# Kernel optimization log

Hardware: AMD Instinct MI355X
Metric: run time of the kernel (lower is better)

## Reference

```python
import jax, jax.numpy as jnp
import numpy as np

B, S, D = 4, 2048, 1024
H, DK, DV = 16, 64, 64
GRAPH_ATTN_BIAS = 2.0
POS_WIN = 4.0
LN_EPS = 1e-6


def setup_inputs() -> dict:
    key = jax.random.key(0)
    ks = jax.random.split(key, 9)
    init = 0.02
    return {
        "q": jax.random.normal(ks[0], (B, S, D), jnp.float32),
        "k": jax.random.normal(ks[1], (B, S, D), jnp.float32),
        "v": jax.random.normal(ks[2], (B, S, D), jnp.float32),
        "Wq": jax.random.normal(ks[3], (D, H * DK), jnp.float32) * init,
        "Wk": jax.random.normal(ks[4], (D, H * DK), jnp.float32) * init,
        "Wv": jax.random.normal(ks[5], (D, H * DV), jnp.float32) * init,
        "Wfc": jax.random.normal(ks[6], (H * DV, D), jnp.float32) * init,
        "gamma": jnp.ones((D,), jnp.float32),
        "beta": jnp.zeros((D,), jnp.float32),
    }


def reference(q, k, v, Wq, Wk, Wv, Wfc, gamma, beta):
    b, sq, d = q.shape
    sk = k.shape[1]
    residual = q
    # projections -> [b, s, h, dk]
    qh = (q @ Wq).reshape(b, sq, H, DK)
    kh = (k @ Wk).reshape(b, sk, H, DK)
    vh = (v @ Wv).reshape(b, sk, H, DV)
    # scaled dot-product scores: [b, h, sq, sk]
    attn = jnp.einsum("bqhd,bkhd->bhqk", qh / jnp.sqrt(jnp.float32(DK)), kh)
    # gaussian graph bias (constant additive logit bias, applied pre-softmax)
    gaussian_w = -0.5 * GRAPH_ATTN_BIAS ** 2 / (0.5 * POS_WIN) ** 2
    attn = attn + gaussian_w
    weights = jax.nn.softmax(attn, axis=-1)
    out = jnp.einsum("bhqk,bkhd->bqhd", weights, vh).reshape(b, sq, H * DV)
    out = out @ Wfc + residual
    # layer norm over last dim, eps=1e-6
    mu = jnp.mean(out, axis=-1, keepdims=True)
    var = jnp.mean((out - mu) ** 2, axis=-1, keepdims=True)
    out = (out - mu) * jax.lax.rsqrt(var + LN_EPS) * gamma + beta
    return out
```

## Files before the change

kernel.cpp:

```cpp
#include <hip/hip_runtime.h>

typedef __attribute__((ext_vector_type(4))) float f32x4;
typedef __attribute__((ext_vector_type(8))) __bf16 bf16x8;

#define MFMA16(a, b, c) __builtin_amdgcn_mfma_f32_16x16x32_bf16(a, b, c, 0, 0, 0)

__device__ __forceinline__ void gload_lds16(const void* g, void* l) {
  __builtin_amdgcn_global_load_lds(
      (const __attribute__((address_space(1))) unsigned int*)g,
      (__attribute__((address_space(3))) unsigned int*)l, 16, 0, 0);
}

__global__ __launch_bounds__(256) void cvt3(
    const float* __restrict__ q, const float* __restrict__ k, const float* __restrict__ v,
    __bf16* __restrict__ qb, __bf16* __restrict__ kb, __bf16* __restrict__ vb) {
  const float* src;
  __bf16* dst;
  if (blockIdx.y == 0) { src = q; dst = qb; }
  else if (blockIdx.y == 1) { src = k; dst = kb; }
  else { src = v; dst = vb; }
  size_t i = ((size_t)blockIdx.x * 256 + threadIdx.x) * 8;
  float4 a = *(const float4*)(src + i);
  float4 b = *(const float4*)(src + i + 4);
  struct alignas(16) B8 { __bf16 h[8]; } ob;
  ob.h[0] = (__bf16)a.x; ob.h[1] = (__bf16)a.y; ob.h[2] = (__bf16)a.z; ob.h[3] = (__bf16)a.w;
  ob.h[4] = (__bf16)b.x; ob.h[5] = (__bf16)b.y; ob.h[6] = (__bf16)b.z; ob.h[7] = (__bf16)b.w;
  *(B8*)(dst + i) = ob;
}

__global__ __launch_bounds__(256) void wtrans(const float* __restrict__ W,
                                              __bf16* __restrict__ Wt) {
  __shared__ float T[64][65];
  int t = threadIdx.x;
  int tc = blockIdx.x, tr = blockIdx.y;
#pragma unroll
  for (int i = 0; i < 4; i++) {
    int r = i * 16 + (t >> 4), c = (t & 15) * 4;
    float4 x = *(const float4*)(W + (size_t)(tr * 64 + r) * 1024 + tc * 64 + c);
    T[r][c] = x.x; T[r][c + 1] = x.y; T[r][c + 2] = x.z; T[r][c + 3] = x.w;
  }
  __syncthreads();
#pragma unroll
  for (int i = 0; i < 4; i++) {
    int r = i * 16 + (t >> 4), c = (t & 15) * 4;
    struct alignas(8) B4 { __bf16 h[4]; } ob;
#pragma unroll
    for (int j = 0; j < 4; j++) ob.h[j] = (__bf16)T[c + j][r];
    *(B4*)(Wt + (size_t)(tc * 64 + r) * 1024 + tr * 64 + c) = ob;
  }
}

template <int MODE>
__global__ __launch_bounds__(256) void gemm_bt(
    const __bf16* __restrict__ A, const __bf16* __restrict__ Bt,
    const float* __restrict__ resid, __bf16* __restrict__ outb,
    float* __restrict__ outf) {
  constexpr int K = 1024;
  __shared__ __align__(16) __bf16 As[128 * 32];
  __shared__ __align__(16) __bf16 Bs[128 * 32];
  int t = threadIdx.x, lane = t & 63, w = t >> 6;
  int l15 = lane & 15, l4 = lane >> 4;
  int m0 = blockIdx.y * 128, n0 = blockIdx.x * 128;
  int wr = w >> 1, wc = w & 1;

  f32x4 z = {0.f, 0.f, 0.f, 0.f};
  f32x4 acc[4][4];
#pragma unroll
  for (int mi = 0; mi < 4; mi++)
#pragma unroll
    for (int ni = 0; ni < 4; ni++) acc[mi][ni] = z;

  int rA = t >> 2, cA = (t & 3) * 8;

  for (int kt = 0; kt < K / 32; ++kt) {
    __syncthreads();
    int k0 = kt * 32;
#pragma unroll
    for (int i = 0; i < 2; i++) {
      gload_lds16(A + (size_t)(m0 + i * 64 + rA) * K + k0 + cA, As + (i * 4 + w) * 512);
      gload_lds16(Bt + (size_t)(n0 + i * 64 + rA) * K + k0 + cA, Bs + (i * 4 + w) * 512);
    }
    __syncthreads();

    bf16x8 af[4], bfr[4];
#pragma unroll
    for (int mi = 0; mi < 4; mi++)
      af[mi] = *(const bf16x8*)(As + (wr * 64 + mi * 16 + l15) * 32 + l4 * 8);
#pragma unroll
    for (int ni = 0; ni < 4; ni++)
      bfr[ni] = *(const bf16x8*)(Bs + (wc * 64 + ni * 16 + l15) * 32 + l4 * 8);
#pragma unroll
    for (int mi = 0; mi < 4; mi++)
#pragma unroll
      for (int ni = 0; ni < 4; ni++)
        acc[mi][ni] = MFMA16(af[mi], bfr[ni], acc[mi][ni]);
  }

#pragma unroll
  for (int mi = 0; mi < 4; mi++)
#pragma unroll
    for (int ni = 0; ni < 4; ni++)
#pragma unroll
      for (int r = 0; r < 4; r++) {
        int row = m0 + wr * 64 + mi * 16 + l4 * 4 + r;
        int col = n0 + wc * 64 + ni * 16 + l15;
        if (MODE == 0) {
          int b = row >> 11, s = row & 2047, h = col >> 6, dk = col & 63;
          outb[(((size_t)b * 16 + h) * 2048 + s) * 64 + dk] = (__bf16)acc[mi][ni][r];
        } else if (MODE == 2) {
          int bh = ((row >> 11) << 4) + (col >> 6);
          outb[((size_t)bh * 64 + (col & 63)) * 2048 + (row & 2047)] = (__bf16)acc[mi][ni][r];
        } else {
          size_t idx = (size_t)row * 1024 + col;
          outf[idx] = acc[mi][ni][r] + resid[idx];
        }
      }
}

__global__ __launch_bounds__(256) void attn_fwd3(
    const __bf16* __restrict__ QH, const __bf16* __restrict__ KH,
    const __bf16* __restrict__ VHt, __bf16* __restrict__ AO) {
  constexpr int S = 2048;
  int bid = blockIdx.x;
  int bh = bid & 63;
  int qt = bid >> 6;
  int t = threadIdx.x, lane = t & 63, w = t >> 6;
  int l15 = lane & 15, l4 = lane >> 4;

  __shared__ __align__(16) __bf16 Ks[2][64 * 64];
  __shared__ __align__(16) __bf16 Vs[2][64 * 64];
  __shared__ __align__(16) __bf16 Ps[4][16 * 64];

  char* myP = (char*)&Ps[w][0];

  const __bf16* Qp = QH + ((size_t)bh * S + qt * 64 + w * 16) * 64;
  const __bf16* Kp = KH + (size_t)bh * S * 64;
  const __bf16* Vp = VHt + (size_t)bh * 64 * S;

  int srow = lane >> 3;
  int sce = ((lane & 7) ^ srow) * 8;

  bf16x8 aq[2];
#pragma unroll
  for (int ks = 0; ks < 2; ks++) {
    bf16x8 x = *(const bf16x8*)(Qp + l15 * 64 + ks * 32 + l4 * 8);
#pragma unroll
    for (int j = 0; j < 8; j++) x[j] = (__bf16)((float)x[j] * 0.125f);
    aq[ks] = x;
  }

  f32x4 z = {0.f, 0.f, 0.f, 0.f};
  f32x4 o[4];
  float mr[4], lr[4];
#pragma unroll
  for (int r = 0; r < 4; r++) { o[r] = z; mr[r] = -1e30f; lr[r] = 0.f; }

#pragma unroll
  for (int i = 0; i < 2; i++) {
    int r = (i * 4 + w) * 8 + srow;
    gload_lds16(Kp + (size_t)r * 64 + sce, &Ks[0][(i * 4 + w) * 512]);
    gload_lds16(Vp + (size_t)r * S + sce, &Vs[0][(i * 4 + w) * 512]);
  }
  __syncthreads();

  for (int kt = 0; kt < 32; ++kt) {
    int cur = kt & 1;
    if (kt < 31) {
#pragma unroll
      for (int i = 0; i < 2; i++) {
        int r = (i * 4 + w) * 8 + srow;
        gload_lds16(Kp + (size_t)((kt + 1) * 64 + r) * 64 + sce,
                    &Ks[cur ^ 1][(i * 4 + w) * 512]);
        gload_lds16(Vp + (size_t)r * S + (kt + 1) * 64 + sce,
                    &Vs[cur ^ 1][(i * 4 + w) * 512]);
      }
    }

    const char* kbuf = (const char*)&Ks[cur][0];
    const char* vbuf = (const char*)&Vs[cur][0];

    bf16x8 kv[2][4];
#pragma unroll
    for (int ks = 0; ks < 2; ks++)
#pragma unroll
      for (int nf = 0; nf < 4; nf++) {
        int row = nf * 16 + l15;
        int cb = (ks * 64 + l4 * 16) ^ ((row & 7) << 4);
        kv[ks][nf] = *(const bf16x8*)(kbuf + row * 128 + cb);
      }

    f32x4 s4[4];
#pragma unroll
    for (int nf = 0; nf < 4; nf++) s4[nf] = z;
#pragma unroll
    for (int ks = 0; ks < 2; ks++)
#pragma unroll
      for (int nf = 0; nf < 4; nf++)
        s4[nf] = MFMA16(aq[ks], kv[ks][nf], s4[nf]);

#pragma unroll
    for (int ks = 0; ks < 2; ks++)
#pragma unroll
      for (int nf = 0; nf < 4; nf++) {
        int row = nf * 16 + l15;
        int cb = (ks * 64 + l4 * 16) ^ ((row & 7) << 4);
        kv[ks][nf] = *(const bf16x8*)(vbuf + row * 128 + cb);
      }

    float pm[4];
#pragma unroll
    for (int r = 0; r < 4; r++) {
      float v0 = fmaxf(fmaxf(s4[0][r], s4[1][r]), fmaxf(s4[2][r], s4[3][r]));
#pragma unroll
      for (int d = 1; d < 16; d <<= 1) v0 = fmaxf(v0, __shfl_xor(v0, d));
      pm[r] = v0;
    }
    float need = fmaxf(fmaxf(pm[0] - mr[0], pm[1] - mr[1]),
                       fmaxf(pm[2] - mr[2], pm[3] - mr[3]));
    if (__any(need > 8.0f)) {
#pragma unroll
      for (int r = 0; r < 4; r++) {
        float mn = fmaxf(mr[r], pm[r]);
        float corr = __expf(mr[r] - mn);
        mr[r] = mn;
        lr[r] *= corr;
#pragma unroll
        for (int nf = 0; nf < 4; nf++) o[nf][r] *= corr;
      }
    }
    float rs[4] = {0.f, 0.f, 0.f, 0.f};
#pragma unroll
    for (int nf = 0; nf < 4; nf++)
#pragma unroll
      for (int r = 0; r < 4; r++) {
        float p = __expf(s4[nf][r] - mr[r]);
        rs[r] += p;
        int rowb = l4 * 4 + r;
        int cb = (nf * 32 + l15 * 2) ^ ((rowb & 7) << 4);
        *(__bf16*)(myP + rowb * 128 + cb) = (__bf16)p;
      }
#pragma unroll
    for (int r = 0; r < 4; r++) {
      float v0 = rs[r];
#pragma unroll
      for (int d = 1; d < 16; d <<= 1) v0 += __shfl_xor(v0, d);
      lr[r] += v0;
    }

    bf16x8 ap[2];
#pragma unroll
    for (int ks = 0; ks < 2; ks++) {
      int cb = (ks * 64 + l4 * 16) ^ ((l15 & 7) << 4);
      ap[ks] = *(const bf16x8*)(myP + l15 * 128 + cb);
    }

#pragma unroll
    for (int ks = 0; ks < 2; ks++)
#pragma unroll
      for (int nf = 0; nf < 4; nf++)
        o[nf] = MFMA16(ap[ks], kv[ks][nf], o[nf]);

    __syncthreads();
  }

  int b = bh >> 4, h = bh & 15;
#pragma unroll
  for (int nf = 0; nf < 4; nf++)
#pragma unroll
    for (int r = 0; r < 4; r++) {
      int row = qt * 64 + w * 16 + l4 * 4 + r;
      int col = h * 64 + nf * 16 + l15;
      AO[((size_t)b * S + row) * 1024 + col] = (__bf16)(o[nf][r] / lr[r]);
    }
}

__global__ __launch_bounds__(256) void ln_inplace(float* __restrict__ X,
                                                  const float* __restrict__ gamma,
                                                  const float* __restrict__ beta) {
  int row = blockIdx.x, t = threadIdx.x;
  int w = t >> 6, lane = t & 63;
  float4 x = *(const float4*)(X + (size_t)row * 1024 + t * 4);
  float s = x.x + x.y + x.z + x.w;
#pragma unroll
  for (int d = 1; d < 64; d <<= 1) s += __shfl_xor(s, d);
  __shared__ float red1[4];
  __shared__ float red2[4];
  if (lane == 0) red1[w] = s;
  __syncthreads();
  float mean = (red1[0] + red1[1] + red1[2] + red1[3]) * (1.0f / 1024.0f);
  float4 d4;
  d4.x = x.x - mean; d4.y = x.y - mean; d4.z = x.z - mean; d4.w = x.w - mean;
  float sq = d4.x * d4.x + d4.y * d4.y + d4.z * d4.z + d4.w * d4.w;
#pragma unroll
  for (int d = 1; d < 64; d <<= 1) sq += __shfl_xor(sq, d);
  if (lane == 0) red2[w] = sq;
  __syncthreads();
  float var = (red2[0] + red2[1] + red2[2] + red2[3]) * (1.0f / 1024.0f);
  float rstd = rsqrtf(var + 1e-6f);
  float4 g = *(const float4*)(gamma + t * 4);
  float4 be = *(const float4*)(beta + t * 4);
  float4 oo;
  oo.x = d4.x * rstd * g.x + be.x;
  oo.y = d4.y * rstd * g.y + be.y;
  oo.z = d4.z * rstd * g.z + be.z;
  oo.w = d4.w * rstd * g.w + be.w;
  *(float4*)(X + (size_t)row * 1024 + t * 4) = oo;
}

extern "C" void kernel_launch(void* const* d_in, const int* in_sizes, int n_in,
                              void* d_out, int out_size, void* d_ws, size_t ws_size,
                              hipStream_t stream) {
  (void)in_sizes; (void)n_in; (void)out_size; (void)ws_size;
  const float* q = (const float*)d_in[0];
  const float* k = (const float*)d_in[1];
  const float* v = (const float*)d_in[2];
  const float* Wq = (const float*)d_in[3];
  const float* Wk = (const float*)d_in[4];
  const float* Wv = (const float*)d_in[5];
  const float* Wfc = (const float*)d_in[6];
  const float* gamma = (const float*)d_in[7];
  const float* beta = (const float*)d_in[8];
  float* out = (float*)d_out;

  const size_t MB = 1ull << 20;
  char* ws = (char*)d_ws;
  __bf16* qb = (__bf16*)(ws + 0 * MB);
  __bf16* kb = (__bf16*)(ws + 16 * MB);
  __bf16* vb = (__bf16*)(ws + 32 * MB);
  __bf16* QH = (__bf16*)(ws + 48 * MB);
  __bf16* KH = (__bf16*)(ws + 64 * MB);
  __bf16* VHt = (__bf16*)(ws + 80 * MB);
  __bf16* Wqt = (__bf16*)(ws + 96 * MB);
  __bf16* Wkt = (__bf16*)(ws + 98 * MB);
  __bf16* Wvt = (__bf16*)(ws + 100 * MB);
  __bf16* Wfct = (__bf16*)(ws + 102 * MB);
  __bf16* AO = qb;

  cvt3<<<dim3(4096, 3), 256, 0, stream>>>(q, k, v, qb, kb, vb);
  wtrans<<<dim3(16, 16), 256, 0, stream>>>(Wq, Wqt);
  wtrans<<<dim3(16, 16), 256, 0, stream>>>(Wk, Wkt);
  wtrans<<<dim3(16, 16), 256, 0, stream>>>(Wv, Wvt);
  wtrans<<<dim3(16, 16), 256, 0, stream>>>(Wfc, Wfct);

  gemm_bt<0><<<dim3(8, 64), 256, 0, stream>>>(qb, Wqt, nullptr, QH, nullptr);
  gemm_bt<0><<<dim3(8, 64), 256, 0, stream>>>(kb, Wkt, nullptr, KH, nullptr);
  gemm_bt<2><<<dim3(8, 64), 256, 0, stream>>>(vb, Wvt, nullptr, VHt, nullptr);

  attn_fwd3<<<2048, 256, 0, stream>>>(QH, KH, VHt, AO);

  gemm_bt<1><<<dim3(8, 64), 256, 0, stream>>>(AO, Wfct, q, nullptr, out);

  ln_inplace<<<8192, 256, 0, stream>>>(out, gamma, beta);
}
```

Baseline: 500.8 us.

## Transpose attention MFMA operands so each lane owns one query row

```diff
diff --git a/kernel.cpp b/kernel.cpp
--- a/kernel.cpp
+++ b/kernel.cpp
@@ -9,6 +9,12 @@
   __builtin_amdgcn_global_load_lds(
       (const __attribute__((address_space(1))) unsigned int*)g,
       (__attribute__((address_space(3))) unsigned int*)l, 16, 0, 0);
+}
+
+__device__ __forceinline__ unsigned int pkbf2(float a, float b) {
+  union { unsigned int u; __bf16 h[2]; } x;
+  x.h[0] = (__bf16)a; x.h[1] = (__bf16)b;
+  return x.u;
 }
 
 __global__ __launch_bounds__(256) void cvt3(
@@ -117,7 +123,7 @@
       }
 }
 
-__global__ __launch_bounds__(256) void attn_fwd3(
+__global__ __launch_bounds__(256) void attn_fwd4(
     const __bf16* __restrict__ QH, const __bf16* __restrict__ KH,
     const __bf16* __restrict__ VHt, __bf16* __restrict__ AO) {
   constexpr int S = 2048;
@@ -129,9 +135,9 @@
 
   __shared__ __align__(16) __bf16 Ks[2][64 * 64];
   __shared__ __align__(16) __bf16 Vs[2][64 * 64];
-  __shared__ __align__(16) __bf16 Ps[4][16 * 64];
-
-  char* myP = (char*)&Ps[w][0];
+  __shared__ __align__(16) char Ps[4][2048];
+
+  char* myP = Ps[w];
 
   const __bf16* Qp = QH + ((size_t)bh * S + qt * 64 + w * 16) * 64;
   const __bf16* Kp = KH + (size_t)bh * S * 64;
@@ -140,20 +146,22 @@
   int srow = lane >> 3;
   int sce = ((lane & 7) ^ srow) * 8;
 
+  const float QSC = 0.125f * 1.44269504088896340736f;
   bf16x8 aq[2];
 #pragma unroll
   for (int ks = 0; ks < 2; ks++) {
     bf16x8 x = *(const bf16x8*)(Qp + l15 * 64 + ks * 32 + l4 * 8);
 #pragma unroll
-    for (int j = 0; j < 8; j++) x[j] = (__bf16)((float)x[j] * 0.125f);
+    for (int j = 0; j < 8; j++) x[j] = (__bf16)((float)x[j] * QSC);
     aq[ks] = x;
   }
 
   f32x4 z = {0.f, 0.f, 0.f, 0.f};
   f32x4 o[4];
-  float mr[4], lr[4];
-#pragma unroll
-  for (int r = 0; r < 4; r++) { o[r] = z; mr[r] = -1e30f; lr[r] = 0.f; }
+#pragma unroll
+  for (int r = 0; r < 4; r++) o[r] = z;
+  float mr = -1e30f, lr = 0.f;
+  const float THR = 11.5417f;
 
 #pragma unroll
   for (int i = 0; i < 2; i++) {
@@ -179,14 +187,14 @@
     const char* kbuf = (const char*)&Ks[cur][0];
     const char* vbuf = (const char*)&Vs[cur][0];
 
-    bf16x8 kv[2][4];
+    bf16x8 kf[2][4];
 #pragma unroll
     for (int ks = 0; ks < 2; ks++)
 #pragma unroll
       for (int nf = 0; nf < 4; nf++) {
         int row = nf * 16 + l15;
         int cb = (ks * 64 + l4 * 16) ^ ((row & 7) << 4);
-        kv[ks][nf] = *(const bf16x8*)(kbuf + row * 128 + cb);
+        kf[ks][nf] = *(const bf16x8*)(kbuf + row * 128 + cb);
       }
 
     f32x4 s4[4];
@@ -196,7 +204,7 @@
     for (int ks = 0; ks < 2; ks++)
 #pragma unroll
       for (int nf = 0; nf < 4; nf++)
-        s4[nf] = MFMA16(aq[ks], kv[ks][nf], s4[nf]);
+        s4[nf] = MFMA16(kf[ks][nf], aq[ks], s4[nf]);
 
 #pragma unroll
     for (int ks = 0; ks < 2; ks++)
@@ -204,74 +212,79 @@
       for (int nf = 0; nf < 4; nf++) {
         int row = nf * 16 + l15;
         int cb = (ks * 64 + l4 * 16) ^ ((row & 7) << 4);
-        kv[ks][nf] = *(const bf16x8*)(vbuf + row * 128 + cb);
+        kf[ks][nf] = *(const bf16x8*)(vbuf + row * 128 + cb);
       }
 
-    float pm[4];
-#pragma unroll
-    for (int r = 0; r < 4; r++) {
-      float v0 = fmaxf(fmaxf(s4[0][r], s4[1][r]), fmaxf(s4[2][r], s4[3][r]));
-#pragma unroll
-      for (int d = 1; d < 16; d <<= 1) v0 = fmaxf(v0, __shfl_xor(v0, d));
-      pm[r] = v0;
-    }
-    float need = fmaxf(fmaxf(pm[0] - mr[0], pm[1] - mr[1]),
-                       fmaxf(pm[2] - mr[2], pm[3] - mr[3]));
-    if (__any(need > 8.0f)) {
-#pragma unroll
-      for (int r = 0; r < 4; r++) {
-        float mn = fmaxf(mr[r], pm[r]);
-        float corr = __expf(mr[r] - mn);
-        mr[r] = mn;
-        lr[r] *= corr;
-#pragma unroll
-        for (int nf = 0; nf < 4; nf++) o[nf][r] *= corr;
-      }
-    }
-    float rs[4] = {0.f, 0.f, 0.f, 0.f};
+    float pm = s4[0][0];
 #pragma unroll
     for (int nf = 0; nf < 4; nf++)
 #pragma unroll
-      for (int r = 0; r < 4; r++) {
-        float p = __expf(s4[nf][r] - mr[r]);
-        rs[r] += p;
-        int rowb = l4 * 4 + r;
-        int cb = (nf * 32 + l15 * 2) ^ ((rowb & 7) << 4);
-        *(__bf16*)(myP + rowb * 128 + cb) = (__bf16)p;
-      }
-#pragma unroll
-    for (int r = 0; r < 4; r++) {
-      float v0 = rs[r];
-#pragma unroll
-      for (int d = 1; d < 16; d <<= 1) v0 += __shfl_xor(v0, d);
-      lr[r] += v0;
-    }
-
-    bf16x8 ap[2];
+      for (int r = 0; r < 4; r++) pm = fmaxf(pm, s4[nf][r]);
+    pm = fmaxf(pm, __shfl_xor(pm, 16));
+    pm = fmaxf(pm, __shfl_xor(pm, 32));
+
+    if (__any(pm - mr > THR)) {
+      float mn = fmaxf(mr, pm);
+      float corr = exp2f(mr - mn);
+      mr = mn;
+      lr *= corr;
+#pragma unroll
+      for (int nf = 0; nf < 4; nf++)
+#pragma unroll
+        for (int r = 0; r < 4; r++) o[nf][r] *= corr;
+    }
+
+    float rs = 0.f;
+    unsigned int pk[4][2];
+#pragma unroll
+    for (int nf = 0; nf < 4; nf++) {
+      float p0 = exp2f(s4[nf][0] - mr);
+      float p1 = exp2f(s4[nf][1] - mr);
+      float p2 = exp2f(s4[nf][2] - mr);
+      float p3 = exp2f(s4[nf][3] - mr);
+      rs += (p0 + p1) + (p2 + p3);
+      pk[nf][0] = pkbf2(p0, p1);
+      pk[nf][1] = pkbf2(p2, p3);
+    }
+    rs += __shfl_xor(rs, 16);
+    rs += __shfl_xor(rs, 32);
+    lr += rs;
+
+    int q = l15;
+#pragma unroll
+    for (int nf = 0; nf < 4; nf++) {
+      int kp = nf * 8 + l4 * 2;
+      int off = q * 128 + ((kp * 4) ^ ((q & 7) << 4) ^ ((q >> 3) << 6));
+      *(uint2*)(myP + off) = make_uint2(pk[nf][0], pk[nf][1]);
+    }
+
+    bf16x8 bp[2];
 #pragma unroll
     for (int ks = 0; ks < 2; ks++) {
-      int cb = (ks * 64 + l4 * 16) ^ ((l15 & 7) << 4);
-      ap[ks] = *(const bf16x8*)(myP + l15 * 128 + cb);
+      int kpb = ks * 16 + l4 * 4;
+      int off = l15 * 128 + ((kpb * 4) ^ ((l15 & 7) << 4) ^ ((l15 >> 3) << 6));
+      bp[ks] = *(const bf16x8*)(myP + off);
     }
 
 #pragma unroll
     for (int ks = 0; ks < 2; ks++)
 #pragma unroll
       for (int nf = 0; nf < 4; nf++)
-        o[nf] = MFMA16(ap[ks], kv[ks][nf], o[nf]);
+        o[nf] = MFMA16(kf[ks][nf], bp[ks], o[nf]);
 
     __syncthreads();
   }
 
   int b = bh >> 4, h = bh & 15;
-#pragma unroll
-  for (int nf = 0; nf < 4; nf++)
-#pragma unroll
-    for (int r = 0; r < 4; r++) {
-      int row = qt * 64 + w * 16 + l4 * 4 + r;
-      int col = h * 64 + nf * 16 + l15;
-      AO[((size_t)b * S + row) * 1024 + col] = (__bf16)(o[nf][r] / lr[r]);
-    }
+  int qrow = qt * 64 + w * 16 + l15;
+  float inv = 1.0f / lr;
+#pragma unroll
+  for (int nf = 0; nf < 4; nf++) {
+    union { ushort4 u4; __bf16 h4[4]; } ob;
+#pragma unroll
+    for (int r = 0; r < 4; r++) ob.h4[r] = (__bf16)(o[nf][r] * inv);
+    *(ushort4*)(AO + ((size_t)b * S + qrow) * 1024 + h * 64 + nf * 16 + l4 * 4) = ob.u4;
+  }
 }
 
 __global__ __launch_bounds__(256) void ln_inplace(float* __restrict__ X,
@@ -346,7 +359,7 @@
   gemm_bt<0><<<dim3(8, 64), 256, 0, stream>>>(kb, Wkt, nullptr, KH, nullptr);
   gemm_bt<2><<<dim3(8, 64), 256, 0, stream>>>(vb, Wvt, nullptr, VHt, nullptr);
 
-  attn_fwd3<<<2048, 256, 0, stream>>>(QH, KH, VHt, AO);
+  attn_fwd4<<<2048, 256, 0, stream>>>(QH, KH, VHt, AO);
 
   gemm_bt<1><<<dim3(8, 64), 256, 0, stream>>>(AO, Wfct, q, nullptr, out);
 
```

Measured after the change: 459.7 us. 8.2% less time.
